# Performance work log

Measured on AMD Instinct MI355X. Metric: run time of the kernel, lower is better.

Reference implementation:

```python
import jax, jax.numpy as jnp
import numpy as np

B, N, F_IN = 8, 1024, 64
HEADS = 8
D = F_IN  # out_features per head (in_features == out_features)


def setup_inputs() -> dict:
    key = jax.random.key(0)
    ks = jax.random.split(key, 5)
    stdv = 1.0 / np.sqrt(F_IN * HEADS)
    h = jax.random.normal(ks[0], (B, N, F_IN), dtype=jnp.float32)
    adj = jnp.ones((B, N, N), dtype=jnp.float32)  # passed but unused by the module
    W = jax.random.uniform(ks[1], (F_IN, D * HEADS), minval=-stdv, maxval=stdv, dtype=jnp.float32)
    a = jax.random.uniform(ks[2], (2 * D, 1), minval=-stdv, maxval=stdv, dtype=jnp.float32)
    out_W = jax.random.normal(ks[3], (D * HEADS, F_IN), dtype=jnp.float32) / np.sqrt(D * HEADS)
    out_b = jnp.zeros((F_IN,), dtype=jnp.float32)
    return {"h": h, "adj": adj, "W": W, "a": a, "out_W": out_W, "out_b": out_b}


def reference(h, adj, W, a, out_W, out_b):
    Bv, Nv, _ = h.shape
    Dh = W.shape[1] // HEADS
    # Wh: [B, N, H, D]
    Wh = (h @ W).reshape(Bv, Nv, HEADS, Dh)
    # Additive attention decomposed: e[b,i,j,h] = leaky_relu(Wh[b,i,h].a_src + Wh[b,j,h].a_dst)
    a_src = jnp.einsum('bnhd,d->bnh', Wh, a[:Dh, 0])
    a_dst = jnp.einsum('bnhd,d->bnh', Wh, a[Dh:, 0])
    e = jax.nn.leaky_relu(a_src[:, :, None, :] + a_dst[:, None, :, :], negative_slope=0.01)  # [B,N,N,H]
    # Module applies softmax over dim=1 (the first node axis i)
    attn = jax.nn.softmax(e, axis=1)  # [B,N,N,H]
    # h_prime[b,i,h,:] = sum_j attn[b,i,j,h] * Wh[b,j,h,:]
    h_prime = jnp.einsum('bijh,bjhd->bihd', attn, Wh).reshape(Bv, Nv, HEADS * Dh)
    return h_prime @ out_W + out_b
```

## Files before the change

kernel.cpp:

```cpp
#include <hip/hip_runtime.h>


#define B_  8
#define N_  1024
#define H_  8
#define D_  64
#define BH_ 64
#define NCH 16
#define CLN 64

__global__ __launch_bounds__(256) void k_wh(
    const float* __restrict__ h, const float* __restrict__ W,
    const float* __restrict__ a,
    float* __restrict__ Wh, float* __restrict__ sArr, float* __restrict__ tArr) {
  __shared__ float hL[16 * 64];
  __shared__ float whL[16 * 512];
  __shared__ float aL[128];
  const int tid = threadIdx.x;
  const int row0 = blockIdx.x * 16;
  const int b = row0 >> 10;
  for (int i = tid; i < 16 * 64; i += 256) hL[i] = h[row0 * 64 + i];
  if (tid < 128) aL[tid] = a[tid];
  __syncthreads();

  float acc0[16], acc1[16];
#pragma unroll
  for (int r = 0; r < 16; ++r) { acc0[r] = 0.f; acc1[r] = 0.f; }
  for (int k = 0; k < 64; ++k) {
    const float w0 = W[k * 512 + tid];
    const float w1 = W[k * 512 + tid + 256];
#pragma unroll
    for (int r = 0; r < 16; ++r) {
      const float hv = hL[r * 64 + k];
      acc0[r] += hv * w0;
      acc1[r] += hv * w1;
    }
  }
  const int hh0 = tid >> 6, d0 = tid & 63;
  const int hh1 = (tid + 256) >> 6;
#pragma unroll
  for (int r = 0; r < 16; ++r) {
    const int n = (row0 + r) & (N_ - 1);
    whL[r * 512 + tid] = acc0[r];
    whL[r * 512 + tid + 256] = acc1[r];
    Wh[((b * H_ + hh0) * N_ + n) * D_ + d0] = acc0[r];
    Wh[((b * H_ + hh1) * N_ + n) * D_ + d0] = acc1[r];
  }
  __syncthreads();
  if (tid < 128) {
    const int r = tid >> 3, hh = tid & 7;
    const int n = (row0 + r) & (N_ - 1);
    float accS = 0.f, accT = 0.f;
    for (int jj = 0; jj < 64; ++jj) {
      const int d = (jj + tid) & 63;
      const float wv = whL[r * 512 + hh * 64 + d];
      accS += wv * aL[d];
      accT += wv * aL[64 + d];
    }
    sArr[(b * H_ + hh) * N_ + n] = accS;
    tArr[(b * H_ + hh) * N_ + n] = accT;
  }
}

__global__ __launch_bounds__(1024) void k_mid(
    const float* __restrict__ sArr, const float* __restrict__ tArr,
    const float* __restrict__ Wh, float* __restrict__ hp) {
  __shared__ float sL[1024], tvL[1024];
  __shared__ int   tiL[1024];
  __shared__ float cum1L[1024], cum001L[1024];
  __shared__ float uL[1024], vL[1024];
  __shared__ float esQ[1024], es001Q[1024];
  __shared__ int   cntL[1025], startL[1025], qList[1024];
  __shared__ float cs1[NCH * 64], cs2[NCH * 64];
  __shared__ float wf1[16], wf2[16];
  __shared__ int   wi1[16];
  const int tid = threadIdx.x, lane = tid & 63, wv = tid >> 6;
  const int bh = blockIdx.x;
  const int b = bh >> 3, hh = bh & 7;

  const float orig_s = sArr[bh * N_ + tid];
  float sv_r = orig_s;
  float tv_r = tArr[bh * N_ + tid];
  int   ti_r = tid;
  cntL[tid] = 0;
  if (tid == 0) cntL[1024] = 0;

  for (int size = 2; size <= 1024; size <<= 1) {
    for (int stride = size >> 1; stride > 0; stride >>= 1) {
      const bool up = ((tid & size) == 0);
      const bool lower = ((tid & stride) == 0);
      float psv, ptv; int pti;
      if (stride >= 64) {
        __syncthreads();
        sL[tid] = sv_r; tvL[tid] = tv_r; tiL[tid] = ti_r;
        __syncthreads();
        psv = sL[tid ^ stride]; ptv = tvL[tid ^ stride]; pti = tiL[tid ^ stride];
      } else {
        psv = __shfl_xor(sv_r, stride);
        ptv = __shfl_xor(tv_r, stride);
        pti = __shfl_xor(ti_r, stride);
      }
      const bool sameDir = (up == lower);
      const bool pLessS = (psv < sv_r);
      if (pLessS == sameDir) sv_r = psv;
      const bool pLessT = (ptv < tv_r) || (ptv == tv_r && pti < ti_r);
      if (pLessT == sameDir) { tv_r = ptv; ti_r = pti; }
    }
  }
  sL[tid] = sv_r; tvL[tid] = tv_r; tiL[tid] = ti_r;

  float c1, c001;
  {
    float a1 = __expf(sv_r), a2 = __expf(0.01f * sv_r);
#pragma unroll
    for (int off = 1; off < 64; off <<= 1) {
      const float x1 = __shfl_up(a1, off);
      const float x2 = __shfl_up(a2, off);
      if (lane >= off) { a1 += x1; a2 += x2; }
    }
    if (lane == 63) { wf1[wv] = a1; wf2[wv] = a2; }
    __syncthreads();
    float o1 = 0.f, o2 = 0.f;
    for (int ww = 0; ww < 16; ++ww) {
      if (ww < wv) { o1 += wf1[ww]; o2 += wf2[ww]; }
    }
    c1 = a1 + o1; c001 = a2 + o2;
  }
  cum1L[tid] = c1; cum001L[tid] = c001;
  __syncthreads();
  const float totalHi = cum1L[1023];

  {
    const float tj = tv_r;
    const float th = -tj;
    int lo = 0, hi = 1024;
    while (lo < hi) { const int mid = (lo + hi) >> 1; if (sL[mid] <= th) lo = mid + 1; else hi = mid; }
    const float S_lo = (lo > 0) ? cum001L[lo - 1] : 0.f;
    const float S_hi = totalHi - ((lo > 0) ? cum1L[lo - 1] : 0.f);
    const float et = __expf(tj), et001 = __expf(0.01f * tj);
    const float Z = et * S_hi + et001 * S_lo;
    uL[tid] = et / Z; vL[tid] = et001 / Z;
  }

  int rk;
  {
    const float th = -orig_s;
    int lo = 0, hi = 1024;
    while (lo < hi) { const int mid = (lo + hi) >> 1; if (tvL[mid] <= th) lo = mid + 1; else hi = mid; }
    rk = lo;
    atomicAdd(&cntL[rk], 1);
    esQ[tid] = __expf(orig_s);
    es001Q[tid] = __expf(0.01f * orig_s);
  }
  __syncthreads();

  {
    const int cown = cntL[tid];
    int a = cown;
#pragma unroll
    for (int off = 1; off < 64; off <<= 1) {
      const int x = __shfl_up(a, off);
      if (lane >= off) a += x;
    }
    if (lane == 63) wi1[wv] = a;
    __syncthreads();
    int o = 0;
    for (int ww = 0; ww < 16; ++ww) {
      if (ww < wv) o += wi1[ww];
    }
    const int incl = a + o;
    startL[tid] = incl - cown;
    if (tid == 1023) startL[1024] = incl;
  }
  __syncthreads();
  cntL[tid] = 0;
  if (tid == 0) cntL[1024] = 0;
  __syncthreads();
  {
    const int pos = startL[rk] + atomicAdd(&cntL[rk], 1);
    qList[pos] = tid;
  }

  {
    float s1 = 0.f, s2 = 0.f;
    for (int k2 = 0; k2 < CLN; ++k2) {
      const int k = wv * CLN + k2;
      const int j = tiL[k];
      const float w = Wh[(bh * N_ + j) * D_ + lane];
      s1 += uL[k] * w;
      s2 += vL[k] * w;
    }
    cs1[wv * 64 + lane] = s1; cs2[wv * 64 + lane] = s2;
  }
  __syncthreads();

  float r1 = 0.f, r2 = 0.f, T1 = 0.f;
  for (int m = 0; m < NCH; ++m) {
    const float v1 = cs1[m * 64 + lane];
    if (m < wv) { r1 += v1; r2 += cs2[m * 64 + lane]; }
    T1 += v1;
  }
  for (int k2 = 0; k2 < CLN; ++k2) {
    const int K = wv * CLN + k2;
    const int qs = startL[K], qe = startL[K + 1];
    for (int q = qs; q < qe; ++q) {
      const int i = qList[q];
      hp[((b * N_ + i) << 9) + (hh << 6) + lane] =
          esQ[i] * (T1 - r1) + es001Q[i] * r2;
    }
    const int j = tiL[K];
    const float w = Wh[(bh * N_ + j) * D_ + lane];
    r1 += uL[K] * w;
    r2 += vL[K] * w;
  }
  if (wv == NCH - 1) {
    const int qs = startL[1024];
    for (int q = qs; q < 1024; ++q) {
      const int i = qList[q];
      hp[((b * N_ + i) << 9) + (hh << 6) + lane] =
          esQ[i] * (T1 - r1) + es001Q[i] * r2;
    }
  }
}

__global__ __launch_bounds__(512) void k_out(
    const float* __restrict__ hp,
    const float* __restrict__ outW, const float* __restrict__ outb,
    float* __restrict__ out) {
  __shared__ float hpL[16 * 512];
  __shared__ float part[8 * 8 * 64];
  const int tid = threadIdx.x;
  const int row0 = blockIdx.x * 16;
  for (int i = tid; i < 16 * 512; i += 512) hpL[i] = hp[row0 * 512 + i];
  __syncthreads();

  const int cc = tid & 63, p = tid >> 6;
  float acc[16];
#pragma unroll
  for (int r = 0; r < 16; ++r) acc[r] = 0.f;
  for (int k = p * 64; k < p * 64 + 64; ++k) {
    const float wvv = outW[k * 64 + cc];
#pragma unroll
    for (int r = 0; r < 16; ++r) acc[r] += hpL[r * 512 + k] * wvv;
  }
  for (int half = 0; half < 2; ++half) {
#pragma unroll
    for (int r = 0; r < 8; ++r) part[(p * 8 + r) * 64 + cc] = acc[half * 8 + r];
    __syncthreads();
    {
      const int r = tid >> 6, c2 = tid & 63;
      float ssum = 0.f;
#pragma unroll
      for (int p2 = 0; p2 < 8; ++p2) ssum += part[(p2 * 8 + r) * 64 + c2];
      out[(row0 + half * 8 + r) * 64 + c2] = outb[c2] + ssum;
    }
    __syncthreads();
  }
}

extern "C" void kernel_launch(void* const* d_in, const int* in_sizes, int n_in,
                              void* d_out, int out_size, void* d_ws, size_t ws_size,
                              hipStream_t stream) {
  const float* h    = (const float*)d_in[0];
  const float* W    = (const float*)d_in[2];
  const float* a    = (const float*)d_in[3];
  const float* outW = (const float*)d_in[4];
  const float* outb = (const float*)d_in[5];
  float* out = (float*)d_out;

  float* ws   = (float*)d_ws;
  float* Wh   = ws;
  float* sArr = Wh + (size_t)BH_ * N_ * D_;
  float* tArr = sArr + BH_ * N_;
  float* hpG  = tArr + BH_ * N_;

  hipLaunchKernelGGL(k_wh,  dim3((B_ * N_) / 16), dim3(256), 0, stream,
                     h, W, a, Wh, sArr, tArr);
  hipLaunchKernelGGL(k_mid, dim3(BH_), dim3(1024), 0, stream,
                     sArr, tArr, Wh, hpG);
  hipLaunchKernelGGL(k_out, dim3((B_ * N_) / 16), dim3(512), 0, stream,
                     hpG, outW, outb, out);
}
```

Before: 167.8 us.

## Split monolithic attention kernel into sort, prefix, and parallel walk kernels

Splits the single per-(batch,head) mid kernel into three launches. The first sorts s and t in separate blocks, doubling the blocks used for sorting. The second computes prefix sums, normalizers and bucket lists and stores them in global workspace. The third runs the sequential sweep as 1024 single-wavefront blocks instead of 16 waves inside 64 large blocks. This is meant to raise GPU occupancy, since the old kernel used only 64 workgroups. The cost is two extra launches and global round-trips for intermediates that previously stayed in shared memory.

```diff
diff --git a/kernel.cpp b/kernel.cpp
--- a/kernel.cpp
+++ b/kernel.cpp
@@ -62,56 +62,90 @@
   }
 }
 
-__global__ __launch_bounds__(1024) void k_mid(
+__global__ __launch_bounds__(1024) void k_sort1(
     const float* __restrict__ sArr, const float* __restrict__ tArr,
-    const float* __restrict__ Wh, float* __restrict__ hp) {
+    float* __restrict__ ssv, float* __restrict__ tsv, int* __restrict__ tsi) {
+  __shared__ float vL[1024];
+  __shared__ int   iL[1024];
+  const int tid = threadIdx.x;
+  const int bh = blockIdx.x >> 1;
+  const bool isT = (blockIdx.x & 1) != 0;
+  if (isT) {
+    float v = tArr[bh * N_ + tid];
+    int   idx = tid;
+    for (int size = 2; size <= 1024; size <<= 1) {
+      for (int stride = size >> 1; stride > 0; stride >>= 1) {
+        const bool up = ((tid & size) == 0);
+        const bool lower = ((tid & stride) == 0);
+        float pv; int pi;
+        if (stride >= 64) {
+          __syncthreads();
+          vL[tid] = v; iL[tid] = idx;
+          __syncthreads();
+          pv = vL[tid ^ stride]; pi = iL[tid ^ stride];
+        } else {
+          pv = __shfl_xor(v, stride);
+          pi = __shfl_xor(idx, stride);
+        }
+        const bool sameDir = (up == lower);
+        const bool pLess = (pv < v) || (pv == v && pi < idx);
+        if (pLess == sameDir) { v = pv; idx = pi; }
+      }
+    }
+    tsv[bh * N_ + tid] = v; tsi[bh * N_ + tid] = idx;
+  } else {
+    float v = sArr[bh * N_ + tid];
+    for (int size = 2; size <= 1024; size <<= 1) {
+      for (int stride = size >> 1; stride > 0; stride >>= 1) {
+        const bool up = ((tid & size) == 0);
+        const bool lower = ((tid & stride) == 0);
+        float pv;
+        if (stride >= 64) {
+          __syncthreads();
+          vL[tid] = v;
+          __syncthreads();
+          pv = vL[tid ^ stride];
+        } else {
+          pv = __shfl_xor(v, stride);
+        }
+        const bool sameDir = (up == lower);
+        if ((pv < v) == sameDir) v = pv;
+      }
+    }
+    ssv[bh * N_ + tid] = v;
+  }
+}
+
+__global__ __launch_bounds__(1024) void k_mid2(
+    const float* __restrict__ sArr,
+    const float* __restrict__ ssv, const float* __restrict__ tsv,
+    const int* __restrict__ tsi, const float* __restrict__ Wh,
+    float* __restrict__ uArr, float* __restrict__ vArr,
+    float* __restrict__ esG, float* __restrict__ es001G,
+    int* __restrict__ startG, int* __restrict__ qListG,
+    float* __restrict__ cOff1, float* __restrict__ cOff2,
+    float* __restrict__ T1G) {
   __shared__ float sL[1024], tvL[1024];
   __shared__ int   tiL[1024];
   __shared__ float cum1L[1024], cum001L[1024];
   __shared__ float uL[1024], vL[1024];
-  __shared__ float esQ[1024], es001Q[1024];
-  __shared__ int   cntL[1025], startL[1025], qList[1024];
+  __shared__ int   cntL[1025], startL[1025];
   __shared__ float cs1[NCH * 64], cs2[NCH * 64];
   __shared__ float wf1[16], wf2[16];
   __shared__ int   wi1[16];
   const int tid = threadIdx.x, lane = tid & 63, wv = tid >> 6;
   const int bh = blockIdx.x;
-  const int b = bh >> 3, hh = bh & 7;
-
-  const float orig_s = sArr[bh * N_ + tid];
-  float sv_r = orig_s;
-  float tv_r = tArr[bh * N_ + tid];
-  int   ti_r = tid;
+  const int base = bh * N_;
+
+  const float sv = ssv[base + tid];
+  const float tj = tsv[base + tid];
+  sL[tid] = sv; tvL[tid] = tj; tiL[tid] = tsi[base + tid];
+  const float orig_s = sArr[base + tid];
   cntL[tid] = 0;
   if (tid == 0) cntL[1024] = 0;
 
-  for (int size = 2; size <= 1024; size <<= 1) {
-    for (int stride = size >> 1; stride > 0; stride >>= 1) {
-      const bool up = ((tid & size) == 0);
-      const bool lower = ((tid & stride) == 0);
-      float psv, ptv; int pti;
-      if (stride >= 64) {
-        __syncthreads();
-        sL[tid] = sv_r; tvL[tid] = tv_r; tiL[tid] = ti_r;
-        __syncthreads();
-        psv = sL[tid ^ stride]; ptv = tvL[tid ^ stride]; pti = tiL[tid ^ stride];
-      } else {
-        psv = __shfl_xor(sv_r, stride);
-        ptv = __shfl_xor(tv_r, stride);
-        pti = __shfl_xor(ti_r, stride);
-      }
-      const bool sameDir = (up == lower);
-      const bool pLessS = (psv < sv_r);
-      if (pLessS == sameDir) sv_r = psv;
-      const bool pLessT = (ptv < tv_r) || (ptv == tv_r && pti < ti_r);
-      if (pLessT == sameDir) { tv_r = ptv; ti_r = pti; }
-    }
-  }
-  sL[tid] = sv_r; tvL[tid] = tv_r; tiL[tid] = ti_r;
-
-  float c1, c001;
-  {
-    float a1 = __expf(sv_r), a2 = __expf(0.01f * sv_r);
+  {
+    float a1 = __expf(sv), a2 = __expf(0.01f * sv);
 #pragma unroll
     for (int off = 1; off < 64; off <<= 1) {
       const float x1 = __shfl_up(a1, off);
@@ -124,14 +158,12 @@
     for (int ww = 0; ww < 16; ++ww) {
       if (ww < wv) { o1 += wf1[ww]; o2 += wf2[ww]; }
     }
-    c1 = a1 + o1; c001 = a2 + o2;
-  }
-  cum1L[tid] = c1; cum001L[tid] = c001;
+    cum1L[tid] = a1 + o1; cum001L[tid] = a2 + o2;
+  }
   __syncthreads();
   const float totalHi = cum1L[1023];
 
   {
-    const float tj = tv_r;
     const float th = -tj;
     int lo = 0, hi = 1024;
     while (lo < hi) { const int mid = (lo + hi) >> 1; if (sL[mid] <= th) lo = mid + 1; else hi = mid; }
@@ -139,7 +171,9 @@
     const float S_hi = totalHi - ((lo > 0) ? cum1L[lo - 1] : 0.f);
     const float et = __expf(tj), et001 = __expf(0.01f * tj);
     const float Z = et * S_hi + et001 * S_lo;
-    uL[tid] = et / Z; vL[tid] = et001 / Z;
+    const float u = et / Z, v = et001 / Z;
+    uL[tid] = u; vL[tid] = v;
+    uArr[base + tid] = u; vArr[base + tid] = v;
   }
 
   int rk;
@@ -149,8 +183,8 @@
     while (lo < hi) { const int mid = (lo + hi) >> 1; if (tvL[mid] <= th) lo = mid + 1; else hi = mid; }
     rk = lo;
     atomicAdd(&cntL[rk], 1);
-    esQ[tid] = __expf(orig_s);
-    es001Q[tid] = __expf(0.01f * orig_s);
+    esG[base + tid] = __expf(orig_s);
+    es001G[base + tid] = __expf(0.01f * orig_s);
   }
   __syncthreads();
 
@@ -170,7 +204,8 @@
     }
     const int incl = a + o;
     startL[tid] = incl - cown;
-    if (tid == 1023) startL[1024] = incl;
+    startG[bh * 1025 + tid] = incl - cown;
+    if (tid == 1023) { startL[1024] = incl; startG[bh * 1025 + 1024] = incl; }
   }
   __syncthreads();
   cntL[tid] = 0;
@@ -178,7 +213,7 @@
   __syncthreads();
   {
     const int pos = startL[rk] + atomicAdd(&cntL[rk], 1);
-    qList[pos] = tid;
+    qListG[base + pos] = tid;
   }
 
   {
@@ -186,7 +221,7 @@
     for (int k2 = 0; k2 < CLN; ++k2) {
       const int k = wv * CLN + k2;
       const int j = tiL[k];
-      const float w = Wh[(bh * N_ + j) * D_ + lane];
+      const float w = Wh[(base + j) * D_ + lane];
       s1 += uL[k] * w;
       s2 += vL[k] * w;
     }
@@ -194,31 +229,60 @@
   }
   __syncthreads();
 
-  float r1 = 0.f, r2 = 0.f, T1 = 0.f;
-  for (int m = 0; m < NCH; ++m) {
-    const float v1 = cs1[m * 64 + lane];
-    if (m < wv) { r1 += v1; r2 += cs2[m * 64 + lane]; }
-    T1 += v1;
-  }
+  {
+    float o1 = 0.f, o2 = 0.f, T1 = 0.f;
+    for (int m = 0; m < NCH; ++m) {
+      const float v1 = cs1[m * 64 + lane];
+      if (m < wv) { o1 += v1; o2 += cs2[m * 64 + lane]; }
+      T1 += v1;
+    }
+    cOff1[(bh * NCH + wv) * 64 + lane] = o1;
+    cOff2[(bh * NCH + wv) * 64 + lane] = o2;
+    if (wv == NCH - 1) T1G[bh * 64 + lane] = T1;
+  }
+}
+
+__global__ __launch_bounds__(64) void k_walk(
+    const float* __restrict__ Wh, const int* __restrict__ tsi,
+    const float* __restrict__ uArr, const float* __restrict__ vArr,
+    const int* __restrict__ startG, const int* __restrict__ qListG,
+    const float* __restrict__ esG, const float* __restrict__ es001G,
+    const float* __restrict__ cOff1, const float* __restrict__ cOff2,
+    const float* __restrict__ T1G, float* __restrict__ hp) {
+  const int blk = blockIdx.x;
+  const int bh = blk >> 4, c = blk & (NCH - 1);
+  const int lane = threadIdx.x;
+  const int b = bh >> 3, hh = bh & 7;
+  const int base = bh * N_;
+
+  float r1 = cOff1[blk * 64 + lane];
+  float r2 = cOff2[blk * 64 + lane];
+  const float T1 = T1G[bh * 64 + lane];
+  const int   tiR = tsi[base + c * CLN + lane];
+  const float uR  = uArr[base + c * CLN + lane];
+  const float vR  = vArr[base + c * CLN + lane];
+  const int   stR = startG[bh * 1025 + c * CLN + lane];
+  const int   stEnd = startG[bh * 1025 + c * CLN + 64];
+
+#pragma unroll 4
   for (int k2 = 0; k2 < CLN; ++k2) {
-    const int K = wv * CLN + k2;
-    const int qs = startL[K], qe = startL[K + 1];
+    const int qs = __shfl(stR, k2);
+    const int qe = (k2 < 63) ? __shfl(stR, k2 + 1) : stEnd;
     for (int q = qs; q < qe; ++q) {
-      const int i = qList[q];
-      hp[((b * N_ + i) << 9) + (hh << 6) + lane] =
-          esQ[i] * (T1 - r1) + es001Q[i] * r2;
-    }
-    const int j = tiL[K];
-    const float w = Wh[(bh * N_ + j) * D_ + lane];
-    r1 += uL[K] * w;
-    r2 += vL[K] * w;
-  }
-  if (wv == NCH - 1) {
-    const int qs = startL[1024];
-    for (int q = qs; q < 1024; ++q) {
-      const int i = qList[q];
-      hp[((b * N_ + i) << 9) + (hh << 6) + lane] =
-          esQ[i] * (T1 - r1) + es001Q[i] * r2;
+      const int i = qListG[base + q];
+      const float es = esG[base + i], es001 = es001G[base + i];
+      hp[((b * N_ + i) << 9) + (hh << 6) + lane] = es * (T1 - r1) + es001 * r2;
+    }
+    const int j = __shfl(tiR, k2);
+    const float w = Wh[(base + j) * D_ + lane];
+    r1 += __shfl(uR, k2) * w;
+    r2 += __shfl(vR, k2) * w;
+  }
+  if (c == NCH - 1) {
+    for (int q = stEnd; q < N_; ++q) {
+      const int i = qListG[base + q];
+      const float es = esG[base + i], es001 = es001G[base + i];
+      hp[((b * N_ + i) << 9) + (hh << 6) + lane] = es * (T1 - r1) + es001 * r2;
     }
   }
 }
@@ -268,16 +332,34 @@
   const float* outb = (const float*)d_in[5];
   float* out = (float*)d_out;
 
-  float* ws   = (float*)d_ws;
-  float* Wh   = ws;
-  float* sArr = Wh + (size_t)BH_ * N_ * D_;
-  float* tArr = sArr + BH_ * N_;
-  float* hpG  = tArr + BH_ * N_;
-
-  hipLaunchKernelGGL(k_wh,  dim3((B_ * N_) / 16), dim3(256), 0, stream,
+  float* ws    = (float*)d_ws;
+  float* Wh    = ws;
+  float* hpG   = Wh + (size_t)BH_ * N_ * D_;
+  float* sArr  = hpG + (size_t)B_ * N_ * 512;
+  float* tArr  = sArr + BH_ * N_;
+  float* ssv   = tArr + BH_ * N_;
+  float* tsv   = ssv + BH_ * N_;
+  int*   tsi   = (int*)(tsv + BH_ * N_);
+  float* uArr  = (float*)(tsi + BH_ * N_);
+  float* vArr  = uArr + BH_ * N_;
+  float* esG   = vArr + BH_ * N_;
+  float* es001G= esG + BH_ * N_;
+  int*   qListG= (int*)(es001G + BH_ * N_);
+  int*   startG= qListG + BH_ * N_;
+  float* cOff1 = (float*)(startG + BH_ * 1025);
+  float* cOff2 = cOff1 + BH_ * NCH * 64;
+  float* T1G   = cOff2 + BH_ * NCH * 64;
+
+  hipLaunchKernelGGL(k_wh,    dim3((B_ * N_) / 16), dim3(256), 0, stream,
                      h, W, a, Wh, sArr, tArr);
-  hipLaunchKernelGGL(k_mid, dim3(BH_), dim3(1024), 0, stream,
-                     sArr, tArr, Wh, hpG);
-  hipLaunchKernelGGL(k_out, dim3((B_ * N_) / 16), dim3(512), 0, stream,
+  hipLaunchKernelGGL(k_sort1, dim3(BH_ * 2), dim3(1024), 0, stream,
+                     sArr, tArr, ssv, tsv, tsi);
+  hipLaunchKernelGGL(k_mid2,  dim3(BH_), dim3(1024), 0, stream,
+                     sArr, ssv, tsv, tsi, Wh,
+                     uArr, vArr, esG, es001G, startG, qListG, cOff1, cOff2, T1G);
+  hipLaunchKernelGGL(k_walk,  dim3(BH_ * NCH), dim3(64), 0, stream,
+                     Wh, tsi, uArr, vArr, startG, qListG, esG, es001G,
+                     cOff1, cOff2, T1G, hpG);
+  hipLaunchKernelGGL(k_out,   dim3((B_ * N_) / 16), dim3(512), 0, stream,
                      hpG, outW, outb, out);
 }
```

After: 190.8 us. +13.7%, slower.
